# Optimization experiments

Hardware: AMD Instinct MI355X
Metric: run time of the kernel (lower is better)

Reference implementation:

```python
import jax, jax.numpy as jnp
import numpy as np

B, C, N, D = 8192, 1000, 2, 512
EPS = 0.1  # epsilon init arg


def setup_inputs() -> dict:
    key = jax.random.key(0)
    kx, kc, kr = jax.random.split(key, 3)
    x = jax.random.normal(kx, (B, D), dtype=jnp.float32)
    centroids = jax.random.uniform(kc, (C, N, D), minval=-1.0, maxval=1.0, dtype=jnp.float32)
    rej_raw = jax.random.uniform(kr, (C * N, D), minval=-1.0, maxval=1.0, dtype=jnp.float32)
    # replicate the __init__ rescaling of the (frozen) rejective centroids
    cmax = jnp.max(jnp.linalg.norm(centroids, axis=-1))
    rej = 2.0 * cmax * rej_raw / (jnp.linalg.norm(rej_raw, axis=-1, keepdims=True) + 1e-16)
    return {"x": x, "centroids": centroids, "rejective_centroids": rej, "return_dists": 1}


def reference(x, centroids, rejective_centroids, return_dists):
    b, d = x.shape
    c, n, _ = centroids.shape
    t = c * n
    # centroid_norm is updated via .data in torch -> detached
    cnorm = jax.lax.stop_gradient(jnp.max(jnp.linalg.norm(centroids, axis=-1)))
    cf = (centroids / (cnorm + 1e-16)).reshape(t, d)  # [T, D] normalized centroids
    # pairwise L2 distances via the expansion identity (no [B,T,D] intermediate)
    x2 = jnp.sum(x * x, axis=-1)          # [B]
    c2 = jnp.sum(cf * cf, axis=-1)        # [T]
    d2 = jnp.maximum(x2[:, None] + c2[None, :] - 2.0 * (x @ cf.T), 0.0)
    dist = jnp.sqrt(d2)                   # [B, T]
    min_dist_class = jnp.min(dist.reshape(b, c, n), axis=2)  # [B, C]
    y = -min_dist_class
    if return_dists:
        idx = jnp.argmin(dist, axis=1)                 # [B]
        closest = cf[idx]                              # [B, D] gathered closest centroid
        r = rejective_centroids                        # [T, D]
        r2 = jnp.sum(r * r, axis=-1)                   # [T]
        xr = x @ r.T                                   # [B, T]
        cr = closest @ r.T                             # [B, T]
        cx = jnp.sum(closest * x, axis=-1)             # [B]
        cl2 = jnp.sum(closest * closest, axis=-1)      # [B]
        # w = closest - r ; b_off = -w . (closest + r)/2 = -0.5(|c|^2 - |r|^2)
        num = jnp.abs(cx[:, None] - xr - 0.5 * (cl2[:, None] - r2[None, :]))
        den = jnp.sqrt(jnp.maximum(cl2[:, None] + r2[None, :] - 2.0 * cr, 0.0)) + 1e-9
        rej_hd = jnp.min(num / den, axis=-1)           # [B]
        return jnp.concatenate([y, rej_hd[:, None]], axis=1)
    min_d = jnp.min(min_dist_class, axis=1)
    removed = jnp.where(min_dist_class == min_d[:, None], jnp.inf, min_dist_class)
    second = jnp.min(removed, axis=1)
    y_bot = -(1.0 - EPS) / (1.0 + EPS) * second
    accept = min_d - EPS * (min_d + second)
    soft = jax.nn.sigmoid(accept)  # ac_temp == 1
    return jnp.concatenate([y, y_bot[:, None], soft[:, None]], axis=1)
```

## Files before the change

kernel.cpp:

```cpp
#include <hip/hip_runtime.h>
#include <math.h>
#include <stdint.h>

#define NB   8192
#define NCLS 1000
#define NT   2000
#define ND   512
#define OUTW 1001

#define OFF_NORM2C 0
#define OFF_R2     2048
#define OFF_X2     4096
#define OFF_SCAL   12288
#define OFF_IDX    12352
#define OFF_CX     20544
#define OFF_CL2    28736

#define NOFF_MIND  36928
#define NOFF_REJP  823360

#define OFF8_MIND  36928
#define OFF8_MINT  102464
#define OFF8_MDOT  168000
#define OFF8_REJP  233536

#define PACKX_B  (8ull<<20)
#define PACKC_B  (24ull<<20)
#define PACKR_B  (28ull<<20)
#define PACKT_B  (32ull<<20)
#define WS_NEED  (48ull<<20)

typedef __attribute__((ext_vector_type(8))) short bf16x8;
typedef __attribute__((ext_vector_type(4))) float f32x4;

__global__ __launch_bounds__(64) void rownorm_kernel(
    const float* __restrict__ cen, const float* __restrict__ rej,
    const float* __restrict__ x, float* __restrict__ ws)
{
    int row = blockIdx.x;
    int lane = threadIdx.x;
    const float* src;
    int dstoff;
    if (row < NT)        { src = cen + (size_t)row * ND;          dstoff = OFF_NORM2C + row; }
    else if (row < 2*NT) { src = rej + (size_t)(row - NT) * ND;   dstoff = OFF_R2 + (row - NT); }
    else                 { src = x   + (size_t)(row - 2*NT) * ND; dstoff = OFF_X2 + (row - 2*NT); }
    float s = 0.f;
#pragma unroll
    for (int k = 0; k < ND / 64; ++k) { float v = src[lane + k * 64]; s += v * v; }
#pragma unroll
    for (int off = 32; off > 0; off >>= 1) s += __shfl_down(s, off);
    if (lane == 0) ws[dstoff] = s;
}

__global__ __launch_bounds__(256) void maxnorm_kernel(float* __restrict__ ws)
{
    __shared__ float sm[256];
    int tid = threadIdx.x;
    float m = 0.f;
    for (int i = tid; i < NT; i += 256) m = fmaxf(m, ws[OFF_NORM2C + i]);
    sm[tid] = m;
    __syncthreads();
    for (int s = 128; s > 0; s >>= 1) {
        if (tid < s) sm[tid] = fmaxf(sm[tid], sm[tid + s]);
        __syncthreads();
    }
    if (tid == 0) {
        float cnorm = sqrtf(sm[0]);
        float inv = 1.f / (cnorm + 1e-16f);
        ws[OFF_SCAL + 0] = cnorm;
        ws[OFF_SCAL + 1] = inv;
        ws[OFF_SCAL + 2] = inv * inv;
    }
}

__device__ __forceinline__ ushort bf16rn(float f){
    uint32_t u = __float_as_uint(f);
    return (ushort)((u + 0x7fffu + ((u >> 16) & 1u)) >> 16);
}

__global__ __launch_bounds__(256) void pack_kernel(const float* __restrict__ src,
    unsigned char* __restrict__ dst, int validRows)
{
    int tid = threadIdx.x;
    int lane = tid & 63;
    int W = blockIdx.x * 4 + (tid >> 6);
    int s  = W >> 4;
    int ks = W & 15;
    int row = s * 16 + (lane & 15);
    int k   = ks * 32 + (lane >> 4) * 8;
    float v[8];
    if (row < validRows) {
        float4 a = *(const float4*)&src[(size_t)row * ND + k];
        float4 b = *(const float4*)&src[(size_t)row * ND + k + 4];
        v[0]=a.x; v[1]=a.y; v[2]=a.z; v[3]=a.w;
        v[4]=b.x; v[5]=b.y; v[6]=b.z; v[7]=b.w;
    } else {
#pragma unroll
        for (int j = 0; j < 8; ++j) v[j] = 0.f;
    }
    union { ushort h[8]; uint4 q; } H, L;
#pragma unroll
    for (int j = 0; j < 8; ++j) {
        ushort hb = bf16rn(v[j]);
        float hf = __uint_as_float(((uint32_t)hb) << 16);
        H.h[j] = hb;
        L.h[j] = bf16rn(v[j] - hf);
    }
    size_t base = ((size_t)(((s >> 3) * 16 + ks) * 16 + (s & 7) * 2)) * 1024;
    *(uint4*)(dst + base + lane * 16)        = H.q;
    *(uint4*)(dst + base + 1024 + lane * 16) = L.q;
}

typedef __attribute__((address_space(3))) unsigned int lds_u32;
typedef const __attribute__((address_space(1))) unsigned int glb_u32;
__device__ __forceinline__ void gload_lds16(const unsigned char* g, unsigned char* l) {
    __builtin_amdgcn_global_load_lds((glb_u32*)g, (lds_u32*)l, 16, 0, 0);
}

template<int PLANES>
__device__ __forceinline__ void stage64(
    const unsigned char* __restrict__ aP2, const unsigned char* __restrict__ bP2,
    int ks, unsigned char* lbuf, int wave, int lane)
{
    if constexpr (PLANES == 3) {
        if (wave < 8) {
#pragma unroll
            for (int j = 0; j < 4; ++j) {
                int gc = wave * 4 + j, s = gc >> 1, pl = gc & 1;
                gload_lds16(aP2 + ((s >> 3) * 16 + ks) * 16384 + ((s & 7) * 2 + pl) * 1024 + lane * 16,
                            lbuf + gc * 1024);
            }
        } else {
#pragma unroll
            for (int j = 0; j < 4; ++j) {
                int gc = (wave - 8) * 4 + j, s = gc >> 1, pl = gc & 1;
                gload_lds16(bP2 + ((s >> 3) * 16 + ks) * 16384 + ((s & 7) * 2 + pl) * 1024 + lane * 16,
                            lbuf + 32768 + gc * 1024);
            }
        }
    } else {
        if (wave < 8) {
#pragma unroll
            for (int j = 0; j < 2; ++j) {
                int cs = wave * 2 + j;
                gload_lds16(aP2 + ((cs >> 3) * 16 + ks) * 16384 + ((cs & 7) * 2) * 1024 + lane * 16,
                            lbuf + cs * 1024);
            }
        } else {
#pragma unroll
            for (int j = 0; j < 2; ++j) {
                int cs = (wave - 8) * 2 + j;
                gload_lds16(bP2 + ((cs >> 3) * 16 + ks) * 16384 + ((cs & 7) * 2) * 1024 + lane * 16,
                            lbuf + 16384 + cs * 1024);
            }
        }
    }
}

#define PASS4(av, bv) do { _Pragma("unroll") \
    for (int qi = 0; qi < 4; ++qi) \
        _Pragma("unroll") \
        for (int ri = 0; ri < 4; ++ri) \
            acc[ri][qi] = __builtin_amdgcn_mfma_f32_16x16x32_bf16( \
                av[ri], bv[qi], acc[ri][qi], 0, 0, 0); \
    } while (0)

template<int PLANES>
__device__ __forceinline__ void compute_step64(
    const unsigned char* __restrict__ cbuf, int lane, int wr, int wc, f32x4 acc[4][4])
{
    if constexpr (PLANES == 3) {
        const unsigned char* aB = cbuf + wr * 8192 + lane * 16;
        const unsigned char* bB = cbuf + 32768 + wc * 8192 + lane * 16;
        bf16x8 ah[4], bh[4];
#pragma unroll
        for (int i = 0; i < 4; ++i) {
            ah[i] = *(const bf16x8*)(aB + i * 2048);
            bh[i] = *(const bf16x8*)(bB + i * 2048);
        }
        PASS4(ah, bh);
        {
            bf16x8 bl[4];
#pragma unroll
            for (int i = 0; i < 4; ++i) bl[i] = *(const bf16x8*)(bB + i * 2048 + 1024);
            PASS4(ah, bl);
        }
        {
            bf16x8 al[4];
#pragma unroll
            for (int i = 0; i < 4; ++i) al[i] = *(const bf16x8*)(aB + i * 2048 + 1024);
            PASS4(al, bh);
        }
    } else {
        const unsigned char* aB = cbuf + wr * 4096 + lane * 16;
        const unsigned char* bB = cbuf + 16384 + wc * 4096 + lane * 16;
        bf16x8 ah[4], bh[4];
#pragma unroll
        for (int i = 0; i < 4; ++i) {
            ah[i] = *(const bf16x8*)(aB + i * 1024);
            bh[i] = *(const bf16x8*)(bB + i * 1024);
        }
        PASS4(ah, bh);
    }
}

#define SCHED_FENCE __builtin_amdgcn_sched_barrier(0)

template<int PLANES>
__device__ __forceinline__ void mfma_core64_pipe(
    const unsigned char* __restrict__ aP2, const unsigned char* __restrict__ bP2,
    unsigned char* lds, int lane, int wave, int wr, int wc, f32x4 acc[4][4])
{
    constexpr int BUF = (PLANES == 3) ? 65536 : 32768;
    stage64<PLANES>(aP2, bP2, 0, lds, wave, lane);
    for (int ks = 0; ks < 16; ++ks) {
        unsigned char* cbuf = lds + (ks & 1) * BUF;
        unsigned char* nbuf = lds + ((ks + 1) & 1) * BUF;
        if (ks < 15) {
            stage64<PLANES>(aP2, bP2, ks + 1, nbuf, wave, lane);
            SCHED_FENCE;
            if constexpr (PLANES == 3) asm volatile("s_waitcnt vmcnt(4)" ::: "memory");
            else                       asm volatile("s_waitcnt vmcnt(2)" ::: "memory");
            SCHED_FENCE;
        } else {
            SCHED_FENCE;
            asm volatile("s_waitcnt vmcnt(0)" ::: "memory");
            SCHED_FENCE;
        }
        __builtin_amdgcn_s_barrier();
        __builtin_amdgcn_s_setprio(1);
        compute_step64<PLANES>(cbuf, lane, wr, wc, acc);
        __builtin_amdgcn_s_setprio(0);
        __builtin_amdgcn_s_barrier();
    }
}

__global__ __launch_bounds__(1024) void dist_mfma_kernel(
    const unsigned char* __restrict__ xpack, const unsigned char* __restrict__ cpack,
    float* __restrict__ out, float* __restrict__ ws)
{
    __shared__ unsigned char lds[2 * 65536];
    int tid = threadIdx.x, lane = tid & 63, wave = tid >> 6;
    int wr = wave >> 2, wc = wave & 3;
    int xb = blockIdx.x, yb = blockIdx.y;
    int b0 = xb * 256, t0base = yb * 256;
    f32x4 acc[4][4];
#pragma unroll
    for (int i = 0; i < 4; ++i)
#pragma unroll
        for (int q = 0; q < 4; ++q) acc[i][q] = (f32x4){0.f, 0.f, 0.f, 0.f};
    mfma_core64_pipe<3>(xpack + (size_t)xb * 524288, cpack + (size_t)yb * 524288,
                        lds, lane, wave, wr, wc, acc);

    float inv  = ws[OFF_SCAL + 1];
    float inv2 = ws[OFF_SCAL + 2];
    int rq = lane >> 4, cidx = lane & 15;
    int seg = yb * 4 + wc;
    float c2q[4]; int tq[4];
#pragma unroll
    for (int qi = 0; qi < 4; ++qi) {
        int t = t0base + wc * 64 + qi * 16 + cidx;
        tq[qi] = t;
        c2q[qi] = (t < NT) ? ws[OFF_NORM2C + t] * inv2 : 0.f;
    }
    unsigned long long* keys = (unsigned long long*)(ws + NOFF_MIND);

#pragma unroll
    for (int ri = 0; ri < 4; ++ri) {
#pragma unroll
        for (int reg = 0; reg < 4; ++reg) {
            int row = b0 + wr * 64 + ri * 16 + rq * 4 + reg;
            float x2 = ws[OFF_X2 + row];
            unsigned long long best = ~0ull;
#pragma unroll
            for (int qi = 0; qi < 4; ++qi) {
                float d2 = fmaxf(x2 + c2q[qi] - 2.f * (acc[ri][qi][reg] * inv), 0.f);
                float d2n = __shfl_xor(d2, 1);
                int t = tq[qi];
                if ((t < NT) && ((cidx & 1) == 0))
                    out[(size_t)row * OUTW + (t >> 1)] = -sqrtf(fminf(d2, d2n));
                if (t < NT) {
                    unsigned long long key =
                        ((unsigned long long)__float_as_uint(d2) << 32) | (unsigned)t;
                    best = best < key ? best : key;
                }
            }
#pragma unroll
            for (int off = 1; off < 16; off <<= 1) {
                unsigned long long o = __shfl_xor(best, off);
                best = best < o ? best : o;
            }
            if (cidx == 0) keys[(size_t)row * 32 + seg] = best;
        }
    }
}

__global__ __launch_bounds__(256) void combine32_kernel(float* __restrict__ ws)
{
    int b = blockIdx.x * 256 + threadIdx.x;
    const unsigned long long* keys = (const unsigned long long*)(ws + NOFF_MIND);
    unsigned long long best = keys[(size_t)b * 32];
#pragma unroll
    for (int s = 1; s < 32; ++s) {
        unsigned long long k = keys[(size_t)b * 32 + s];
        best = best < k ? best : k;
    }
    int bt = (int)(best & 0xffffffffull);
    float d2 = __uint_as_float((unsigned)(best >> 32));
    float c2 = ws[OFF_NORM2C + bt] * ws[OFF_SCAL + 2];
    float x2 = ws[OFF_X2 + b];
    ((int*)ws)[OFF_IDX + b] = bt;
    ws[OFF_CX + b] = 0.5f * (x2 + c2 - d2);
    ws[OFF_CL2 + b] = c2;
}

#define LOADA1(buf, ks_) do { _Pragma("unroll") \
    for (int i = 0; i < 4; ++i) { \
        buf[i] = *(const bf16x8*)(aB + (ks_) * 16384 + i * 2048); \
    } } while (0)
#define LOADB1(buf, ks_) do { _Pragma("unroll") \
    for (int i = 0; i < 4; ++i) { \
        buf[i] = *(const bf16x8*)(bB + (ks_) * 16384 + i * 2048); \
    } } while (0)
#define COMPUTE1(av, bv) PASS4(av, bv)

__device__ __forceinline__ void mfma_core_db1(
    const unsigned char* __restrict__ aP, const unsigned char* __restrict__ bP,
    int lane, int wr, int wc, f32x4 acc[4][4])
{
    const unsigned char* aB = aP + wr * 8192 + lane * 16;
    const unsigned char* bB = bP + wc * 8192 + lane * 16;
    bf16x8 a0[4], a1[4], b0[4], b1[4];
    LOADA1(a0, 0); LOADB1(b0, 0);
    for (int ks = 0; ks < 16; ks += 2) {
        LOADA1(a1, ks + 1); LOADB1(b1, ks + 1);
        COMPUTE1(a0, b0);
        if (ks + 2 < 16) { LOADA1(a0, ks + 2); LOADB1(b0, ks + 2); }
        COMPUTE1(a1, b1);
    }
}

__global__ __launch_bounds__(256, 2) void table_mfma_kernel(
    const unsigned char* __restrict__ cpack, const unsigned char* __restrict__ rpack,
    float* __restrict__ table, const float* __restrict__ ws)
{
    int tid = threadIdx.x, lane = tid & 63, wave = tid >> 6;
    int wr = wave >> 1, wc = wave & 1;
    int c0 = blockIdx.x * 128, t0base = blockIdx.y * 128;
    f32x4 acc[4][4];
#pragma unroll
    for (int i = 0; i < 4; ++i)
#pragma unroll
        for (int q = 0; q < 4; ++q) acc[i][q] = (f32x4){0.f, 0.f, 0.f, 0.f};
    mfma_core_db1(cpack + (size_t)blockIdx.x * 262144, rpack + (size_t)blockIdx.y * 262144,
                  lane, wr, wc, acc);

    float inv  = ws[OFF_SCAL + 1];
    float inv2 = ws[OFF_SCAL + 2];
    int rq = lane >> 4, cidx = lane & 15;
    float r2q[4]; int tq[4];
#pragma unroll
    for (int qi = 0; qi < 4; ++qi) {
        int t = t0base + wc * 64 + qi * 16 + cidx;
        tq[qi] = t;
        r2q[qi] = (t < NT) ? ws[OFF_R2 + t] : 0.f;
    }
#pragma unroll
    for (int ri = 0; ri < 4; ++ri) {
#pragma unroll
        for (int reg = 0; reg < 4; ++reg) {
            int c = c0 + wr * 64 + ri * 16 + rq * 4 + reg;
            if (c < NT) {
                float cl2c = ws[OFF_NORM2C + c] * inv2;
#pragma unroll
                for (int qi = 0; qi < 4; ++qi) {
                    int t = tq[qi];
                    if (t < NT) {
                        float cfr = acc[ri][qi][reg] * inv;
                        float den = sqrtf(fmaxf(cl2c + r2q[qi] - 2.f * cfr, 0.f)) + 1e-9f;
                        table[(size_t)c * 2048 + t] = 1.f / den;
                    }
                }
            }
        }
    }
}

__global__ __launch_bounds__(1024) void xr_mfma_kernel(
    const unsigned char* __restrict__ xpack, const unsigned char* __restrict__ rpack,
    const float* __restrict__ table, float* __restrict__ ws)
{
    __shared__ unsigned char lds[2 * 32768];
    int tid = threadIdx.x, lane = tid & 63, wave = tid >> 6;
    int wr = wave >> 2, wc = wave & 3;
    int xb = blockIdx.x, yb = blockIdx.y;
    int b0 = xb * 256, t0base = yb * 256;
    f32x4 acc[4][4];
#pragma unroll
    for (int i = 0; i < 4; ++i)
#pragma unroll
        for (int q = 0; q < 4; ++q) acc[i][q] = (f32x4){0.f, 0.f, 0.f, 0.f};
    mfma_core64_pipe<1>(xpack + (size_t)xb * 524288, rpack + (size_t)yb * 524288,
                        lds, lane, wave, wr, wc, acc);

    int rq = lane >> 4, cidx = lane & 15;
    int seg = yb * 4 + wc;
    float r2q[4]; int tq[4];
#pragma unroll
    for (int qi = 0; qi < 4; ++qi) {
        int t = t0base + wc * 64 + qi * 16 + cidx;
        tq[qi] = t;
        r2q[qi] = (t < NT) ? ws[OFF_R2 + t] : 0.f;
    }
#pragma unroll
    for (int ri = 0; ri < 4; ++ri) {
#pragma unroll
        for (int reg = 0; reg < 4; ++reg) {
            int row = b0 + wr * 64 + ri * 16 + rq * 4 + reg;
            int idx = ((const int*)ws)[OFF_IDX + row];
            float cx  = ws[OFF_CX + row];
            float cl2 = ws[OFF_CL2 + row];
            const float* trow = table + (size_t)idx * 2048;
            float mv = INFINITY;
#pragma unroll
            for (int qi = 0; qi < 4; ++qi) {
                int t = tq[qi];
                if (t < NT) {
                    float num = fabsf(cx - acc[ri][qi][reg] - 0.5f * (cl2 - r2q[qi]));
                    mv = fminf(mv, num * trow[t]);
                }
            }
#pragma unroll
            for (int off = 1; off < 16; off <<= 1) mv = fminf(mv, __shfl_xor(mv, off));
            if (cidx == 0) ws[NOFF_REJP + (size_t)row * 32 + seg] = mv;
        }
    }
}

__global__ __launch_bounds__(256) void rejcombine32_kernel(
    const float* __restrict__ ws, float* __restrict__ out)
{
    int b = blockIdx.x * 256 + threadIdx.x;
    float bd = ws[NOFF_REJP + (size_t)b * 32];
#pragma unroll
    for (int s = 1; s < 32; ++s) bd = fminf(bd, ws[NOFF_REJP + (size_t)b * 32 + s]);
    out[(size_t)b * OUTW + NCLS] = bd;
}

#define BK   32
#define LDST 68

__global__ __launch_bounds__(256) void dist_kernel(
    const float* __restrict__ x, const float* __restrict__ cen,
    float* __restrict__ out, float* __restrict__ ws)
{
    __shared__ float Xs[BK][LDST];
    __shared__ float Cs[BK][LDST];
    __shared__ float red_d[64][17];
    __shared__ int   red_t[64][17];
    __shared__ float red_x[64][17];

    int tid = threadIdx.x;
    int tx = tid & 15, ty = tid >> 4;
    int b0 = blockIdx.x * 64;
    int tseg0 = blockIdx.y * 256;
    int tseg1 = min(tseg0 + 256, NT);

    float inv  = ws[OFF_SCAL + 1];
    float inv2 = ws[OFF_SCAL + 2];
    float x2v[4];
#pragma unroll
    for (int i = 0; i < 4; ++i) x2v[i] = ws[OFF_X2 + b0 + ty * 4 + i];

    int lr = tid >> 2;
    int lc = (tid & 3) * 8;

    float mind[4], mdot[4];
    int mint[4];
#pragma unroll
    for (int i = 0; i < 4; ++i) { mind[i] = INFINITY; mint[i] = 0x7fffffff; mdot[i] = 0.f; }

    for (int t0 = tseg0; t0 < tseg1; t0 += 64) {
        float acc[4][4];
#pragma unroll
        for (int i = 0; i < 4; ++i)
#pragma unroll
            for (int jj = 0; jj < 4; ++jj) acc[i][jj] = 0.f;

        for (int k0 = 0; k0 < ND; k0 += BK) {
            {
                const float4 v0 = *(const float4*)&x[(size_t)(b0 + lr) * ND + k0 + lc];
                const float4 v1 = *(const float4*)&x[(size_t)(b0 + lr) * ND + k0 + lc + 4];
                Xs[lc + 0][lr] = v0.x; Xs[lc + 1][lr] = v0.y; Xs[lc + 2][lr] = v0.z; Xs[lc + 3][lr] = v0.w;
                Xs[lc + 4][lr] = v1.x; Xs[lc + 5][lr] = v1.y; Xs[lc + 6][lr] = v1.z; Xs[lc + 7][lr] = v1.w;
            }
            {
                int tr = t0 + lr;
                float4 v0 = make_float4(0.f, 0.f, 0.f, 0.f), v1 = v0;
                if (tr < NT) {
                    v0 = *(const float4*)&cen[(size_t)tr * ND + k0 + lc];
                    v1 = *(const float4*)&cen[(size_t)tr * ND + k0 + lc + 4];
                }
                Cs[lc + 0][lr] = v0.x; Cs[lc + 1][lr] = v0.y; Cs[lc + 2][lr] = v0.z; Cs[lc + 3][lr] = v0.w;
                Cs[lc + 4][lr] = v1.x; Cs[lc + 5][lr] = v1.y; Cs[lc + 6][lr] = v1.z; Cs[lc + 7][lr] = v1.w;
            }
            __syncthreads();
#pragma unroll
            for (int kk = 0; kk < BK; ++kk) {
                float4 av = *(const float4*)&Xs[kk][ty * 4];
                float4 bv = *(const float4*)&Cs[kk][tx * 4];
                float a[4] = {av.x, av.y, av.z, av.w};
                float bb[4] = {bv.x, bv.y, bv.z, bv.w};
#pragma unroll
                for (int i = 0; i < 4; ++i)
#pragma unroll
                    for (int jj = 0; jj < 4; ++jj)
                        acc[i][jj] = fmaf(a[i], bb[jj], acc[i][jj]);
            }
            __syncthreads();
        }

        float distv[4][4];
#pragma unroll
        for (int jj = 0; jj < 4; ++jj) {
            int t = t0 + tx * 4 + jj;
            bool valid = (t < NT);
            float c2 = valid ? ws[OFF_NORM2C + t] * inv2 : 0.f;
#pragma unroll
            for (int i = 0; i < 4; ++i) {
                float dsc = acc[i][jj] * inv;
                float d2 = x2v[i] + c2 - 2.f * dsc;
                float dd = sqrtf(fmaxf(d2, 0.f));
                distv[i][jj] = dd;
                if (valid && (dd < mind[i])) { mind[i] = dd; mint[i] = t; mdot[i] = dsc; }
            }
        }
#pragma unroll
        for (int jp = 0; jp < 2; ++jp) {
            int t = t0 + tx * 4 + jp * 2;
            if (t < NT) {
                int cls = t >> 1;
#pragma unroll
                for (int i = 0; i < 4; ++i) {
                    out[(size_t)(b0 + ty * 4 + i) * OUTW + cls] =
                        -fminf(distv[i][jp * 2], distv[i][jp * 2 + 1]);
                }
            }
        }
    }

#pragma unroll
    for (int i = 0; i < 4; ++i) {
        red_d[ty * 4 + i][tx] = mind[i];
        red_t[ty * 4 + i][tx] = mint[i];
        red_x[ty * 4 + i][tx] = mdot[i];
    }
    __syncthreads();
    if (tid < 64) {
        float bd = red_d[tid][0]; int bt = red_t[tid][0]; float bx = red_x[tid][0];
        for (int q = 1; q < 16; ++q) {
            float d = red_d[tid][q]; int tt = red_t[tid][q];
            if (d < bd || (d == bd && tt < bt)) { bd = d; bt = tt; bx = red_x[tid][q]; }
        }
        int b = b0 + tid;
        int s = blockIdx.y;
        ws[OFF8_MIND + b * 8 + s] = bd;
        ((int*)ws)[OFF8_MINT + b * 8 + s] = bt;
        ws[OFF8_MDOT + b * 8 + s] = bx;
    }
}

__global__ __launch_bounds__(256) void combine_kernel(float* __restrict__ ws)
{
    int b = blockIdx.x * 256 + threadIdx.x;
    float bd = ws[OFF8_MIND + b * 8];
    int   bt = ((int*)ws)[OFF8_MINT + b * 8];
    float bx = ws[OFF8_MDOT + b * 8];
#pragma unroll
    for (int s = 1; s < 8; ++s) {
        float d = ws[OFF8_MIND + b * 8 + s];
        int  tt = ((int*)ws)[OFF8_MINT + b * 8 + s];
        if (d < bd || (d == bd && tt < bt)) { bd = d; bt = tt; bx = ws[OFF8_MDOT + b * 8 + s]; }
    }
    ((int*)ws)[OFF_IDX + b] = bt;
    ws[OFF_CX + b] = bx;
    ws[OFF_CL2 + b] = ws[OFF_NORM2C + bt] * ws[OFF_SCAL + 2];
}

__global__ __launch_bounds__(256) void rej_kernel(
    const float* __restrict__ x, const float* __restrict__ cen,
    const float* __restrict__ rej, float* __restrict__ ws)
{
    __shared__ float Xs[BK][LDST];
    __shared__ float Rs[BK][LDST];
    __shared__ float Ls[BK][LDST];
    __shared__ int idxL[64];
    __shared__ float red_d[64][17];

    int tid = threadIdx.x;
    int tx = tid & 15, ty = tid >> 4;
    int b0 = blockIdx.x * 64;
    int tseg0 = blockIdx.y * 256;
    int tseg1 = min(tseg0 + 256, NT);
    float inv = ws[OFF_SCAL + 1];

    if (tid < 64) idxL[tid] = ((int*)ws)[OFF_IDX + b0 + tid];
    float cxv[4], cl2v[4];
#pragma unroll
    for (int i = 0; i < 4; ++i) {
        cxv[i]  = ws[OFF_CX  + b0 + ty * 4 + i];
        cl2v[i] = ws[OFF_CL2 + b0 + ty * 4 + i];
    }
    __syncthreads();

    int lr = tid >> 2, lc = (tid & 3) * 8;
    int myrow = idxL[lr];

    float minv[4] = {INFINITY, INFINITY, INFINITY, INFINITY};

    for (int t0 = tseg0; t0 < tseg1; t0 += 64) {
        float xr[4][4], cr[4][4];
#pragma unroll
        for (int i = 0; i < 4; ++i)
#pragma unroll
            for (int jj = 0; jj < 4; ++jj) { xr[i][jj] = 0.f; cr[i][jj] = 0.f; }

        for (int k0 = 0; k0 < ND; k0 += BK) {
            {
                const float4 v0 = *(const float4*)&x[(size_t)(b0 + lr) * ND + k0 + lc];
                const float4 v1 = *(const float4*)&x[(size_t)(b0 + lr) * ND + k0 + lc + 4];
                Xs[lc + 0][lr] = v0.x; Xs[lc + 1][lr] = v0.y; Xs[lc + 2][lr] = v0.z; Xs[lc + 3][lr] = v0.w;
                Xs[lc + 4][lr] = v1.x; Xs[lc + 5][lr] = v1.y; Xs[lc + 6][lr] = v1.z; Xs[lc + 7][lr] = v1.w;
            }
            {
                const float4 v0 = *(const float4*)&cen[(size_t)myrow * ND + k0 + lc];
                const float4 v1 = *(const float4*)&cen[(size_t)myrow * ND + k0 + lc + 4];
                Ls[lc + 0][lr] = v0.x * inv; Ls[lc + 1][lr] = v0.y * inv;
                Ls[lc + 2][lr] = v0.z * inv; Ls[lc + 3][lr] = v0.w * inv;
                Ls[lc + 4][lr] = v1.x * inv; Ls[lc + 5][lr] = v1.y * inv;
                Ls[lc + 6][lr] = v1.z * inv; Ls[lc + 7][lr] = v1.w * inv;
            }
            {
                int tr = t0 + lr;
                float4 v0 = make_float4(0.f, 0.f, 0.f, 0.f), v1 = v0;
                if (tr < NT) {
                    v0 = *(const float4*)&rej[(size_t)tr * ND + k0 + lc];
                    v1 = *(const float4*)&rej[(size_t)tr * ND + k0 + lc + 4];
                }
                Rs[lc + 0][lr] = v0.x; Rs[lc + 1][lr] = v0.y; Rs[lc + 2][lr] = v0.z; Rs[lc + 3][lr] = v0.w;
                Rs[lc + 4][lr] = v1.x; Rs[lc + 5][lr] = v1.y; Rs[lc + 6][lr] = v1.z; Rs[lc + 7][lr] = v1.w;
            }
            __syncthreads();
#pragma unroll
            for (int kk = 0; kk < BK; ++kk) {
                float4 av = *(const float4*)&Xs[kk][ty * 4];
                float4 lv = *(const float4*)&Ls[kk][ty * 4];
                float4 rv = *(const float4*)&Rs[kk][tx * 4];
                float a[4] = {av.x, av.y, av.z, av.w};
                float l[4] = {lv.x, lv.y, lv.z, lv.w};
                float r[4] = {rv.x, rv.y, rv.z, rv.w};
#pragma unroll
                for (int i = 0; i < 4; ++i)
#pragma unroll
                    for (int jj = 0; jj < 4; ++jj) {
                        xr[i][jj] = fmaf(a[i], r[jj], xr[i][jj]);
                        cr[i][jj] = fmaf(l[i], r[jj], cr[i][jj]);
                    }
            }
            __syncthreads();
        }

#pragma unroll
        for (int jj = 0; jj < 4; ++jj) {
            int t = t0 + tx * 4 + jj;
            if (t < NT) {
                float r2 = ws[OFF_R2 + t];
#pragma unroll
                for (int i = 0; i < 4; ++i) {
                    float num = fabsf(cxv[i] - xr[i][jj] - 0.5f * (cl2v[i] - r2));
                    float den = sqrtf(fmaxf(cl2v[i] + r2 - 2.f * cr[i][jj], 0.f)) + 1e-9f;
                    minv[i] = fminf(minv[i], num / den);
                }
            }
        }
    }

#pragma unroll
    for (int i = 0; i < 4; ++i) red_d[ty * 4 + i][tx] = minv[i];
    __syncthreads();
    if (tid < 64) {
        float bd = red_d[tid][0];
        for (int q = 1; q < 16; ++q) bd = fminf(bd, red_d[tid][q]);
        ws[OFF8_REJP + (size_t)(b0 + tid) * 8 + blockIdx.y] = bd;
    }
}

__global__ __launch_bounds__(256) void rejcombine_kernel(
    const float* __restrict__ ws, float* __restrict__ out)
{
    int b = blockIdx.x * 256 + threadIdx.x;
    float bd = ws[OFF8_REJP + b * 8];
#pragma unroll
    for (int s = 1; s < 8; ++s) bd = fminf(bd, ws[OFF8_REJP + b * 8 + s]);
    out[(size_t)b * OUTW + NCLS] = bd;
}

extern "C" void kernel_launch(void* const* d_in, const int* in_sizes, int n_in,
                              void* d_out, int out_size, void* d_ws, size_t ws_size,
                              hipStream_t stream)
{
    const float* x   = (const float*)d_in[0];
    const float* cen = (const float*)d_in[1];
    const float* rej = (const float*)d_in[2];
    float* out = (float*)d_out;
    float* ws  = (float*)d_ws;
    unsigned char* wsb = (unsigned char*)d_ws;

    rownorm_kernel<<<2 * NT + NB, 64, 0, stream>>>(cen, rej, x, ws);
    maxnorm_kernel<<<1, 256, 0, stream>>>(ws);

    if (ws_size >= WS_NEED) {
        pack_kernel<<<2048, 256, 0, stream>>>(x,   wsb + PACKX_B, NB);
        pack_kernel<<<512,  256, 0, stream>>>(cen, wsb + PACKC_B, NT);
        pack_kernel<<<512,  256, 0, stream>>>(rej, wsb + PACKR_B, NT);
        dist_mfma_kernel<<<dim3(32, 8), 1024, 0, stream>>>(wsb + PACKX_B, wsb + PACKC_B, out, ws);
        combine32_kernel<<<32, 256, 0, stream>>>(ws);
        table_mfma_kernel<<<dim3(16, 16), 256, 0, stream>>>(wsb + PACKC_B, wsb + PACKR_B,
                                                            (float*)(wsb + PACKT_B), ws);
        xr_mfma_kernel<<<dim3(32, 8), 1024, 0, stream>>>(wsb + PACKX_B, wsb + PACKR_B,
                                                         (float*)(wsb + PACKT_B), ws);
        rejcombine32_kernel<<<32, 256, 0, stream>>>(ws, out);
    } else {
        dist_kernel<<<dim3(NB / 64, 8), 256, 0, stream>>>(x, cen, out, ws);
        combine_kernel<<<NB / 256, 256, 0, stream>>>(ws);
        rej_kernel<<<dim3(NB / 64, 8), 256, 0, stream>>>(x, cen, rej, ws);
        rejcombine_kernel<<<NB / 256, 256, 0, stream>>>(ws, out);
    }
}
```

Measured before the change: 161.9 us.

## Store reciprocal-distance table in bf16 and stage two k-steps per barrier in xr kernel

The 1/den lookup table is now written and read as bf16 instead of fp32, which halves the gather traffic in the xr epilogue. The xr GEMM loop is restructured to stage two k-slices per double-buffer stage in a 64KB buffer, so it runs 8 barrier rounds instead of 16, with setprio applied around each MFMA pass. The cost is lower precision in the rejection distance (bf16 reciprocal) and twice the LDS per block for the xr kernel.

```diff
diff --git a/kernel.cpp b/kernel.cpp
--- a/kernel.cpp
+++ b/kernel.cpp
@@ -117,45 +117,7 @@
     __builtin_amdgcn_global_load_lds((glb_u32*)g, (lds_u32*)l, 16, 0, 0);
 }
 
-template<int PLANES>
-__device__ __forceinline__ void stage64(
-    const unsigned char* __restrict__ aP2, const unsigned char* __restrict__ bP2,
-    int ks, unsigned char* lbuf, int wave, int lane)
-{
-    if constexpr (PLANES == 3) {
-        if (wave < 8) {
-#pragma unroll
-            for (int j = 0; j < 4; ++j) {
-                int gc = wave * 4 + j, s = gc >> 1, pl = gc & 1;
-                gload_lds16(aP2 + ((s >> 3) * 16 + ks) * 16384 + ((s & 7) * 2 + pl) * 1024 + lane * 16,
-                            lbuf + gc * 1024);
-            }
-        } else {
-#pragma unroll
-            for (int j = 0; j < 4; ++j) {
-                int gc = (wave - 8) * 4 + j, s = gc >> 1, pl = gc & 1;
-                gload_lds16(bP2 + ((s >> 3) * 16 + ks) * 16384 + ((s & 7) * 2 + pl) * 1024 + lane * 16,
-                            lbuf + 32768 + gc * 1024);
-            }
-        }
-    } else {
-        if (wave < 8) {
-#pragma unroll
-            for (int j = 0; j < 2; ++j) {
-                int cs = wave * 2 + j;
-                gload_lds16(aP2 + ((cs >> 3) * 16 + ks) * 16384 + ((cs & 7) * 2) * 1024 + lane * 16,
-                            lbuf + cs * 1024);
-            }
-        } else {
-#pragma unroll
-            for (int j = 0; j < 2; ++j) {
-                int cs = (wave - 8) * 2 + j;
-                gload_lds16(bP2 + ((cs >> 3) * 16 + ks) * 16384 + ((cs & 7) * 2) * 1024 + lane * 16,
-                            lbuf + 16384 + cs * 1024);
-            }
-        }
-    }
-}
+#define SCHED_FENCE __builtin_amdgcn_sched_barrier(0)
 
 #define PASS4(av, bv) do { _Pragma("unroll") \
     for (int qi = 0; qi < 4; ++qi) \
@@ -165,62 +127,65 @@
                 av[ri], bv[qi], acc[ri][qi], 0, 0, 0); \
     } while (0)
 
-template<int PLANES>
-__device__ __forceinline__ void compute_step64(
+__device__ __forceinline__ void stage_dist(
+    const unsigned char* __restrict__ aP2, const unsigned char* __restrict__ bP2,
+    int ks, unsigned char* lbuf, int wave, int lane)
+{
+    if (wave < 8) {
+#pragma unroll
+        for (int j = 0; j < 4; ++j) {
+            int gc = wave * 4 + j, s = gc >> 1, pl = gc & 1;
+            gload_lds16(aP2 + ((s >> 3) * 16 + ks) * 16384 + ((s & 7) * 2 + pl) * 1024 + lane * 16,
+                        lbuf + gc * 1024);
+        }
+    } else {
+#pragma unroll
+        for (int j = 0; j < 4; ++j) {
+            int gc = (wave - 8) * 4 + j, s = gc >> 1, pl = gc & 1;
+            gload_lds16(bP2 + ((s >> 3) * 16 + ks) * 16384 + ((s & 7) * 2 + pl) * 1024 + lane * 16,
+                        lbuf + 32768 + gc * 1024);
+        }
+    }
+}
+
+__device__ __forceinline__ void compute_dist(
     const unsigned char* __restrict__ cbuf, int lane, int wr, int wc, f32x4 acc[4][4])
 {
-    if constexpr (PLANES == 3) {
-        const unsigned char* aB = cbuf + wr * 8192 + lane * 16;
-        const unsigned char* bB = cbuf + 32768 + wc * 8192 + lane * 16;
-        bf16x8 ah[4], bh[4];
-#pragma unroll
-        for (int i = 0; i < 4; ++i) {
-            ah[i] = *(const bf16x8*)(aB + i * 2048);
-            bh[i] = *(const bf16x8*)(bB + i * 2048);
-        }
-        PASS4(ah, bh);
-        {
-            bf16x8 bl[4];
-#pragma unroll
-            for (int i = 0; i < 4; ++i) bl[i] = *(const bf16x8*)(bB + i * 2048 + 1024);
-            PASS4(ah, bl);
-        }
-        {
-            bf16x8 al[4];
-#pragma unroll
-            for (int i = 0; i < 4; ++i) al[i] = *(const bf16x8*)(aB + i * 2048 + 1024);
-            PASS4(al, bh);
-        }
-    } else {
-        const unsigned char* aB = cbuf + wr * 4096 + lane * 16;
-        const unsigned char* bB = cbuf + 16384 + wc * 4096 + lane * 16;
-        bf16x8 ah[4], bh[4];
-#pragma unroll
-        for (int i = 0; i < 4; ++i) {
-            ah[i] = *(const bf16x8*)(aB + i * 1024);
-            bh[i] = *(const bf16x8*)(bB + i * 1024);
-        }
-        PASS4(ah, bh);
-    }
-}
-
-#define SCHED_FENCE __builtin_amdgcn_sched_barrier(0)
-
-template<int PLANES>
-__device__ __forceinline__ void mfma_core64_pipe(
+    const unsigned char* aB = cbuf + wr * 8192 + lane * 16;
+    const unsigned char* bB = cbuf + 32768 + wc * 8192 + lane * 16;
+    bf16x8 ah[4], bh[4];
+#pragma unroll
+    for (int i = 0; i < 4; ++i) {
+        ah[i] = *(const bf16x8*)(aB + i * 2048);
+        bh[i] = *(const bf16x8*)(bB + i * 2048);
+    }
+    PASS4(ah, bh);
+    {
+        bf16x8 bl[4];
+#pragma unroll
+        for (int i = 0; i < 4; ++i) bl[i] = *(const bf16x8*)(bB + i * 2048 + 1024);
+        PASS4(ah, bl);
+    }
+    {
+        bf16x8 al[4];
+#pragma unroll
+        for (int i = 0; i < 4; ++i) al[i] = *(const bf16x8*)(aB + i * 2048 + 1024);
+        PASS4(al, bh);
+    }
+}
+
+__device__ __forceinline__ void mfma_core_dist(
     const unsigned char* __restrict__ aP2, const unsigned char* __restrict__ bP2,
     unsigned char* lds, int lane, int wave, int wr, int wc, f32x4 acc[4][4])
 {
-    constexpr int BUF = (PLANES == 3) ? 65536 : 32768;
-    stage64<PLANES>(aP2, bP2, 0, lds, wave, lane);
+    stage_dist(aP2, bP2, 0, lds, wave, lane);
     for (int ks = 0; ks < 16; ++ks) {
-        unsigned char* cbuf = lds + (ks & 1) * BUF;
-        unsigned char* nbuf = lds + ((ks + 1) & 1) * BUF;
+        unsigned char* cbuf = lds + (ks & 1) * 65536;
+        unsigned char* nbuf = lds + ((ks + 1) & 1) * 65536;
         if (ks < 15) {
-            stage64<PLANES>(aP2, bP2, ks + 1, nbuf, wave, lane);
+            stage_dist(aP2, bP2, ks + 1, nbuf, wave, lane);
             SCHED_FENCE;
-            if constexpr (PLANES == 3) asm volatile("s_waitcnt vmcnt(4)" ::: "memory");
-            else                       asm volatile("s_waitcnt vmcnt(2)" ::: "memory");
+            asm volatile("s_waitcnt vmcnt(4)" ::: "memory");
             SCHED_FENCE;
         } else {
             SCHED_FENCE;
@@ -229,8 +194,68 @@
         }
         __builtin_amdgcn_s_barrier();
         __builtin_amdgcn_s_setprio(1);
-        compute_step64<PLANES>(cbuf, lane, wr, wc, acc);
+        compute_dist(cbuf, lane, wr, wc, acc);
         __builtin_amdgcn_s_setprio(0);
+        __builtin_amdgcn_s_barrier();
+    }
+}
+
+__device__ __forceinline__ void stage_xr(
+    const unsigned char* __restrict__ aP2, const unsigned char* __restrict__ bP2,
+    int ks2, unsigned char* lbuf, int wave, int lane)
+{
+#pragma unroll
+    for (int j = 0; j < 4; ++j) {
+        int q = (wave & 7) * 4 + j;
+        int sub = q >> 4, cs = q & 15;
+        int ks = ks2 * 2 + sub;
+        const unsigned char* src = (wave < 8)
+            ? aP2 + ((cs >> 3) * 16 + ks) * 16384 + ((cs & 7) * 2) * 1024 + lane * 16
+            : bP2 + ((cs >> 3) * 16 + ks) * 16384 + ((cs & 7) * 2) * 1024 + lane * 16;
+        unsigned char* dst = lbuf + (wave < 8 ? 0 : 32768) + sub * 16384 + cs * 1024;
+        gload_lds16(src, dst);
+    }
+}
+
+__device__ __forceinline__ void compute_xr(
+    const unsigned char* __restrict__ cbuf, int lane, int wr, int wc, f32x4 acc[4][4])
+{
+#pragma unroll
+    for (int sub = 0; sub < 2; ++sub) {
+        const unsigned char* aB = cbuf + sub * 16384 + wr * 4096 + lane * 16;
+        const unsigned char* bB = cbuf + 32768 + sub * 16384 + wc * 4096 + lane * 16;
+        bf16x8 ah[4], bh[4];
+#pragma unroll
+        for (int i = 0; i < 4; ++i) {
+            ah[i] = *(const bf16x8*)(aB + i * 1024);
+            bh[i] = *(const bf16x8*)(bB + i * 1024);
+        }
+        __builtin_amdgcn_s_setprio(1);
+        PASS4(ah, bh);
+        __builtin_amdgcn_s_setprio(0);
+    }
+}
+
+__device__ __forceinline__ void mfma_core_xr(
+    const unsigned char* __restrict__ aP2, const unsigned char* __restrict__ bP2,
+    unsigned char* lds, int lane, int wave, int wr, int wc, f32x4 acc[4][4])
+{
+    stage_xr(aP2, bP2, 0, lds, wave, lane);
+    for (int ks2 = 0; ks2 < 8; ++ks2) {
+        unsigned char* cbuf = lds + (ks2 & 1) * 65536;
+        unsigned char* nbuf = lds + ((ks2 + 1) & 1) * 65536;
+        if (ks2 < 7) {
+            stage_xr(aP2, bP2, ks2 + 1, nbuf, wave, lane);
+            SCHED_FENCE;
+            asm volatile("s_waitcnt vmcnt(4)" ::: "memory");
+            SCHED_FENCE;
+        } else {
+            SCHED_FENCE;
+            asm volatile("s_waitcnt vmcnt(0)" ::: "memory");
+            SCHED_FENCE;
+        }
+        __builtin_amdgcn_s_barrier();
+        compute_xr(cbuf, lane, wr, wc, acc);
         __builtin_amdgcn_s_barrier();
     }
 }
@@ -249,8 +274,8 @@
     for (int i = 0; i < 4; ++i)
 #pragma unroll
         for (int q = 0; q < 4; ++q) acc[i][q] = (f32x4){0.f, 0.f, 0.f, 0.f};
-    mfma_core64_pipe<3>(xpack + (size_t)xb * 524288, cpack + (size_t)yb * 524288,
-                        lds, lane, wave, wr, wc, acc);
+    mfma_core_dist(xpack + (size_t)xb * 524288, cpack + (size_t)yb * 524288,
+                   lds, lane, wave, wr, wc, acc);
 
     float inv  = ws[OFF_SCAL + 1];
     float inv2 = ws[OFF_SCAL + 2];
@@ -322,7 +347,6 @@
     for (int i = 0; i < 4; ++i) { \
         buf[i] = *(const bf16x8*)(bB + (ks_) * 16384 + i * 2048); \
     } } while (0)
-#define COMPUTE1(av, bv) PASS4(av, bv)
 
 __device__ __forceinline__ void mfma_core_db1(
     const unsigned char* __restrict__ aP, const unsigned char* __restrict__ bP,
@@ -334,15 +358,15 @@
     LOADA1(a0, 0); LOADB1(b0, 0);
     for (int ks = 0; ks < 16; ks += 2) {
         LOADA1(a1, ks + 1); LOADB1(b1, ks + 1);
-        COMPUTE1(a0, b0);
+        PASS4(a0, b0);
         if (ks + 2 < 16) { LOADA1(a0, ks + 2); LOADB1(b0, ks + 2); }
-        COMPUTE1(a1, b1);
+        PASS4(a1, b1);
     }
 }
 
 __global__ __launch_bounds__(256, 2) void table_mfma_kernel(
     const unsigned char* __restrict__ cpack, const unsigned char* __restrict__ rpack,
-    float* __restrict__ table, const float* __restrict__ ws)
+    ushort* __restrict__ table, const float* __restrict__ ws)
 {
     int tid = threadIdx.x, lane = tid & 63, wave = tid >> 6;
     int wr = wave >> 1, wc = wave & 1;
@@ -378,7 +402,7 @@
                     if (t < NT) {
                         float cfr = acc[ri][qi][reg] * inv;
                         float den = sqrtf(fmaxf(cl2c + r2q[qi] - 2.f * cfr, 0.f)) + 1e-9f;
-                        table[(size_t)c * 2048 + t] = 1.f / den;
+                        table[(size_t)c * 2048 + t] = bf16rn(1.f / den);
                     }
                 }
             }
@@ -388,9 +412,9 @@
 
 __global__ __launch_bounds__(1024) void xr_mfma_kernel(
     const unsigned char* __restrict__ xpack, const unsigned char* __restrict__ rpack,
-    const float* __restrict__ table, float* __restrict__ ws)
-{
-    __shared__ unsigned char lds[2 * 32768];
+    const ushort* __restrict__ table, float* __restrict__ ws)
+{
+    __shared__ unsigned char lds[2 * 65536];
     int tid = threadIdx.x, lane = tid & 63, wave = tid >> 6;
     int wr = wave >> 2, wc = wave & 3;
     int xb = blockIdx.x, yb = blockIdx.y;
@@ -400,8 +424,8 @@
     for (int i = 0; i < 4; ++i)
 #pragma unroll
         for (int q = 0; q < 4; ++q) acc[i][q] = (f32x4){0.f, 0.f, 0.f, 0.f};
-    mfma_core64_pipe<1>(xpack + (size_t)xb * 524288, rpack + (size_t)yb * 524288,
-                        lds, lane, wave, wr, wc, acc);
+    mfma_core_xr(xpack + (size_t)xb * 524288, rpack + (size_t)yb * 524288,
+                 lds, lane, wave, wr, wc, acc);
 
     int rq = lane >> 4, cidx = lane & 15;
     int seg = yb * 4 + wc;
@@ -420,14 +444,18 @@
             int idx = ((const int*)ws)[OFF_IDX + row];
             float cx  = ws[OFF_CX + row];
             float cl2 = ws[OFF_CL2 + row];
-            const float* trow = table + (size_t)idx * 2048;
+            const ushort* trow = table + (size_t)idx * 2048;
+            float tv[4];
+#pragma unroll
+            for (int qi = 0; qi < 4; ++qi)
+                tv[qi] = (tq[qi] < NT)
+                    ? __uint_as_float(((uint32_t)trow[tq[qi]]) << 16) : 0.f;
             float mv = INFINITY;
 #pragma unroll
             for (int qi = 0; qi < 4; ++qi) {
-                int t = tq[qi];
-                if (t < NT) {
+                if (tq[qi] < NT) {
                     float num = fabsf(cx - acc[ri][qi][reg] - 0.5f * (cl2 - r2q[qi]));
-                    mv = fminf(mv, num * trow[t]);
+                    mv = fminf(mv, num * tv[qi]);
                 }
             }
 #pragma unroll
@@ -726,9 +754,9 @@
         dist_mfma_kernel<<<dim3(32, 8), 1024, 0, stream>>>(wsb + PACKX_B, wsb + PACKC_B, out, ws);
         combine32_kernel<<<32, 256, 0, stream>>>(ws);
         table_mfma_kernel<<<dim3(16, 16), 256, 0, stream>>>(wsb + PACKC_B, wsb + PACKR_B,
-                                                            (float*)(wsb + PACKT_B), ws);
+                                                            (ushort*)(wsb + PACKT_B), ws);
         xr_mfma_kernel<<<dim3(32, 8), 1024, 0, stream>>>(wsb + PACKX_B, wsb + PACKR_B,
-                                                         (float*)(wsb + PACKT_B), ws);
+                                                         (const ushort*)(wsb + PACKT_B), ws);
         rejcombine32_kernel<<<32, 256, 0, stream>>>(ws, out);
     } else {
         dist_kernel<<<dim3(NB / 64, 8), 256, 0, stream>>>(x, cen, out, ws);
```

Result: faster. 153.0 us, median of 2 (-5.5%).
